# Kernel optimization log

Hardware: AMD Instinct MI355X
Metric: run time of the kernel (lower is better)

The kernel has to match this reference:

```python
import jax, jax.numpy as jnp
import numpy as np

N = 100000          # nodes
E = 1600000         # edges (before self loops)
F_IN = 128          # num_features
HID = 16            # hidden_channels (per head)
HEADS = 4
NCLS = 16           # num_classes (per head)
NEG_SLOPE = 0.2     # PyG GATv2Conv default


def gatv2_conv(x, src, dst, w_l, w_r, att, bias, heads, out_ch):
    """PyG GATv2Conv (concat=True, add_self_loops handled by caller).
    x: [N, Fin]; src/dst: [E']; w_l/w_r: [Fin, heads*out_ch]; att: [heads, out_ch].
    """
    n = x.shape[0]
    x_l = (x @ w_l).reshape(n, heads, out_ch)  # source-side transform
    x_r = (x @ w_r).reshape(n, heads, out_ch)  # target-side transform
    # per-edge attention logits: a^T LeakyReLU(x_l[j] + x_r[i])
    e = jax.nn.leaky_relu(x_l[src] + x_r[dst], NEG_SLOPE)   # [E', H, C]
    logits = jnp.einsum('ehc,hc->eh', e, att)               # [E', H]
    # segment softmax over incoming edges of each dst node
    m = jax.ops.segment_max(logits, dst, num_segments=n)    # [N, H]
    a = jnp.exp(logits - m[dst])
    denom = jax.ops.segment_sum(a, dst, num_segments=n)     # [N, H]
    alpha = a / denom[dst]                                  # self loops => denom > 0
    out = jax.ops.segment_sum(alpha[:, :, None] * x_l[src], dst, num_segments=n)
    return out.reshape(n, heads * out_ch) + bias


def setup_inputs() -> dict:
    key = jax.random.key(0)
    ks = jax.random.split(key, 10)
    x = jax.random.normal(ks[0], (N, F_IN), dtype=jnp.float32)
    edge_index = jax.random.randint(ks[1], (2, E), 0, N, dtype=jnp.int64)
    d1 = HEADS * HID   # 64
    s1 = 1.0 / np.sqrt(F_IN)
    s2 = 1.0 / np.sqrt(d1)
    return {
        'x': x,
        'edge_index': edge_index,
        'w_l1': jax.random.normal(ks[2], (F_IN, d1), dtype=jnp.float32) * s1,
        'w_r1': jax.random.normal(ks[3], (F_IN, d1), dtype=jnp.float32) * s1,
        'att1': jax.random.normal(ks[4], (HEADS, HID), dtype=jnp.float32) * s2,
        'b1': jnp.zeros((d1,), dtype=jnp.float32),
        'w_l2': jax.random.normal(ks[5], (d1, HEADS * NCLS), dtype=jnp.float32) * s2,
        'w_r2': jax.random.normal(ks[6], (d1, HEADS * NCLS), dtype=jnp.float32) * s2,
        'att2': jax.random.normal(ks[7], (HEADS, NCLS), dtype=jnp.float32) * (1.0 / np.sqrt(NCLS)),
        'b2': jnp.zeros((HEADS * NCLS,), dtype=jnp.float32),
    }


def reference(x, edge_index, w_l1, w_r1, att1, b1, w_l2, w_r2, att2, b2):
    # add self loops (PyG GATv2Conv default add_self_loops=True)
    loop = jnp.arange(N, dtype=edge_index.dtype)
    src = jnp.concatenate([edge_index[0], loop])
    dst = jnp.concatenate([edge_index[1], loop])
    h = gatv2_conv(x, src, dst, w_l1, w_r1, att1, b1, HEADS, HID)
    h = jax.nn.relu(h)
    out = gatv2_conv(h, src, dst, w_l2, w_r2, att2, b2, HEADS, NCLS)
    return out
```

## Files before the change

### kernel.cpp

```cpp
#include <hip/hip_runtime.h>
#include <hip/hip_fp16.h>

#define FIN 128
#define BSH 9
#define BMASK ((1 << BSH) - 1)
#define CHUNK 8192
#define BCAP 10240

typedef _Float16 half4 __attribute__((ext_vector_type(4)));
typedef _Float16 h2v __attribute__((ext_vector_type(2)));
typedef float f32x4 __attribute__((ext_vector_type(4)));

static __device__ __forceinline__ float xor1_add(float p) {
  const int sw = __builtin_amdgcn_mov_dpp(__builtin_bit_cast(int, p), 0xB1,
                                          0xF, 0xF, true);
  return p + __builtin_bit_cast(float, sw);
}

template<int K, bool FP32IN>
__global__ __launch_bounds__(256) void gemm_mfma(
    const void* __restrict__ xin, const float* __restrict__ wl,
    const float* __restrict__ wr, __half* __restrict__ outl,
    __half* __restrict__ outr, int n) {
  constexpr int WSTR = K + 4;
  __shared__ _Float16 Wt[128 * WSTR];
  const int tid = threadIdx.x;
  for (int i4 = tid; i4 < K * 16; i4 += 256) {
    const int k = i4 >> 4, c0 = (i4 & 15) << 2;
    const float4 vl = *(const float4*)&wl[k * 64 + c0];
    const float4 vr = *(const float4*)&wr[k * 64 + c0];
    Wt[(c0 + 0) * WSTR + k] = (_Float16)vl.x;
    Wt[(c0 + 1) * WSTR + k] = (_Float16)vl.y;
    Wt[(c0 + 2) * WSTR + k] = (_Float16)vl.z;
    Wt[(c0 + 3) * WSTR + k] = (_Float16)vl.w;
    Wt[(c0 + 64) * WSTR + k] = (_Float16)vr.x;
    Wt[(c0 + 65) * WSTR + k] = (_Float16)vr.y;
    Wt[(c0 + 66) * WSTR + k] = (_Float16)vr.z;
    Wt[(c0 + 67) * WSTR + k] = (_Float16)vr.w;
  }
  __syncthreads();
  const int lane = tid & 63;
  const int wv = tid >> 6;
  const int r0 = blockIdx.x * 64 + wv * 16;
  const int rowc = min(r0 + (lane & 15), n - 1);
  const int kgrp = (lane >> 4) << 2;
  const int col16 = lane & 15;
  f32x4 acc[8];
#pragma unroll
  for (int cf = 0; cf < 8; ++cf) acc[cf] = {0.f, 0.f, 0.f, 0.f};
  for (int ks = 0; ks < K / 16; ++ks) {
    const int kb = ks * 16 + kgrp;
    half4 a;
    if (FP32IN) {
      const float4 av =
          *(const float4*)((const float*)xin + (size_t)rowc * K + kb);
      a = {(_Float16)av.x, (_Float16)av.y, (_Float16)av.z, (_Float16)av.w};
    } else {
      a = *(const half4*)((const __half*)xin + (size_t)rowc * K + kb);
    }
#pragma unroll
    for (int cf = 0; cf < 8; ++cf) {
      const half4 b = *(const half4*)&Wt[(cf * 16 + col16) * WSTR + kb];
      acc[cf] = __builtin_amdgcn_mfma_f32_16x16x16f16(a, b, acc[cf], 0, 0, 0);
    }
  }
  const int crow0 = r0 + ((lane >> 4) << 2);
#pragma unroll
  for (int cf = 0; cf < 8; ++cf) {
    const int c = cf * 16 + col16;
    __half* outp = (c < 64) ? outl : outr;
    const int cc = c & 63;
#pragma unroll
    for (int r = 0; r < 4; ++r) {
      const int rr = crow0 + r;
      if (rr < n) outp[(size_t)rr * 64 + cc] = (__half)acc[cf][r];
    }
  }
}

__global__ __launch_bounds__(256) void binpass(
    const int* __restrict__ src, const int* __restrict__ dst, int E, int ET,
    int NB, int* __restrict__ gcursor, unsigned* __restrict__ sorted_val) {
  __shared__ unsigned lval[CHUNK];
  __shared__ unsigned short lrank[CHUNK];
  __shared__ unsigned char lb[CHUNK];
  __shared__ int c1[256], base[256];
  const int tid = threadIdx.x;
  c1[tid] = 0;
  __syncthreads();
  const int e0 = blockIdx.x * CHUNK;

#define BPROC(idx_, s_, d_)                                                  \
  {                                                                          \
    const int b_ = (d_) >> BSH;                                              \
    lval[idx_] = (unsigned)(s_) | ((unsigned)((d_) & BMASK) << 17);          \
    lb[idx_] = (unsigned char)b_;                                            \
    lrank[idx_] = (unsigned short)atomicAdd(&c1[b_], 1);                     \
  }

#pragma unroll
  for (int j = 0; j < CHUNK / 1024; ++j) {
    const int q = tid + 256 * j;
    const int e = e0 + 4 * q;
    if (e + 3 < E) {
      const int4 s4 = *(const int4*)&src[e];
      const int4 d4 = *(const int4*)&dst[e];
      BPROC(4 * q + 0, s4.x, d4.x);
      BPROC(4 * q + 1, s4.y, d4.y);
      BPROC(4 * q + 2, s4.z, d4.z);
      BPROC(4 * q + 3, s4.w, d4.w);
    } else {
#pragma unroll
      for (int t = 0; t < 4; ++t) {
        const int ee = e + t;
        const int idx = 4 * q + t;
        if (ee < ET) {
          int s, d;
          if (ee < E) {
            s = src[ee];
            d = dst[ee];
          } else {
            s = d = ee - E;
          }
          BPROC(idx, s, d);
        } else {
          lb[idx] = 255;
        }
      }
    }
  }
#undef BPROC
  __syncthreads();
  if (tid < NB && c1[tid] > 0)
    base[tid] = tid * BCAP + atomicAdd(&gcursor[tid], c1[tid]);
  __syncthreads();
#pragma unroll
  for (int j = 0; j < CHUNK / 256; ++j) {
    const int idx = tid + 256 * j;
    const int b = lb[idx];
    if (b != 255) sorted_val[base[b] + lrank[idx]] = lval[idx];
  }
}

__global__ __launch_bounds__(256) void scatter_gemm1(
    const int* __restrict__ gcursor, const unsigned* __restrict__ sorted_val,
    int n, int* __restrict__ ssrc, int2* __restrict__ off2,
    const float* __restrict__ x, const float* __restrict__ wl,
    const float* __restrict__ wr, __half* __restrict__ outl,
    __half* __restrict__ outr, int NB,
    const float* __restrict__ att1, const float* __restrict__ att2,
    __half* __restrict__ att1h, __half* __restrict__ att2h) {
  __shared__ __align__(16) char smem[49152];
  const int tid = threadIdx.x;

  if (blockIdx.x == 0 && tid < 64) {
    att1h[tid] = (__half)(att1[tid] * 1.44269504f);
    att2h[tid] = (__half)(att2[tid] * 1.44269504f);
  }

  if (blockIdx.x < (unsigned)NB) {
    int* cnt = (int*)smem;
    int* sa = cnt + 512;
    int* sb = sa + 512;
    int* cur = sb + 512;
    int* buf = cur + 512;
    const int b = blockIdx.x;
    const int node0 = b << BSH;
    const int nn = min(512, n - node0);
    const int rbase = b * BCAP;
    const int rlen = gcursor[b];
    for (int j = tid; j < 512; j += 256) cnt[j] = 0;
    __syncthreads();
    for (int i = tid; i < rlen; i += 256)
      atomicAdd(&cnt[sorted_val[rbase + i] >> 17], 1);
    __syncthreads();
    for (int j = tid; j < 512; j += 256) sa[j] = cnt[j];
    __syncthreads();
    int* pin = sa;
    int* pout = sb;
    for (int off = 1; off < 512; off <<= 1) {
      for (int j = tid; j < 512; j += 256)
        pout[j] = pin[j] + (j >= off ? pin[j - off] : 0);
      __syncthreads();
      int* t = pin;
      pin = pout;
      pout = t;
    }
    for (int j = tid; j < 512; j += 256) {
      const int excl = pin[j] - cnt[j];
      cur[j] = excl;
      if (j < nn) off2[node0 + j] = make_int2(rbase + excl, rbase + pin[j]);
    }
    __syncthreads();
    if (rlen <= BCAP) {
      for (int i = tid; i < rlen; i += 256) {
        const unsigned v = sorted_val[rbase + i];
        const int p = atomicAdd(&cur[v >> 17], 1);
        buf[p] = (int)(v & 0x1FFFFu);
      }
      __syncthreads();
      for (int i = tid; i < rlen; i += 256) ssrc[rbase + i] = buf[i];
    } else {
      for (int i = tid; i < rlen; i += 256) {
        const unsigned v = sorted_val[rbase + i];
        const int p = atomicAdd(&cur[v >> 17], 1);
        ssrc[rbase + p] = (int)(v & 0x1FFFFu);
      }
    }
  } else {
    constexpr int K = 128;
    constexpr int WSTR = K + 4;
    _Float16* Wt = (_Float16*)smem;
    for (int i4 = tid; i4 < K * 16; i4 += 256) {
      const int k = i4 >> 4, c0 = (i4 & 15) << 2;
      const float4 vl = *(const float4*)&wl[k * 64 + c0];
      const float4 vr = *(const float4*)&wr[k * 64 + c0];
      Wt[(c0 + 0) * WSTR + k] = (_Float16)vl.x;
      Wt[(c0 + 1) * WSTR + k] = (_Float16)vl.y;
      Wt[(c0 + 2) * WSTR + k] = (_Float16)vl.z;
      Wt[(c0 + 3) * WSTR + k] = (_Float16)vl.w;
      Wt[(c0 + 64) * WSTR + k] = (_Float16)vr.x;
      Wt[(c0 + 65) * WSTR + k] = (_Float16)vr.y;
      Wt[(c0 + 66) * WSTR + k] = (_Float16)vr.z;
      Wt[(c0 + 67) * WSTR + k] = (_Float16)vr.w;
    }
    __syncthreads();
    const int lane = tid & 63;
    const int wv = tid >> 6;
    const int r0 = (blockIdx.x - NB) * 64 + wv * 16;
    const int rowc = min(r0 + (lane & 15), n - 1);
    const int kgrp = (lane >> 4) << 2;
    const int col16 = lane & 15;
    f32x4 acc[8];
#pragma unroll
    for (int cf = 0; cf < 8; ++cf) acc[cf] = {0.f, 0.f, 0.f, 0.f};
    for (int ks = 0; ks < K / 16; ++ks) {
      const int kb = ks * 16 + kgrp;
      const float4 av = *(const float4*)&x[(size_t)rowc * K + kb];
      const half4 a = {(_Float16)av.x, (_Float16)av.y, (_Float16)av.z,
                       (_Float16)av.w};
#pragma unroll
      for (int cf = 0; cf < 8; ++cf) {
        const half4 bb = *(const half4*)&Wt[(cf * 16 + col16) * WSTR + kb];
        acc[cf] = __builtin_amdgcn_mfma_f32_16x16x16f16(a, bb, acc[cf], 0, 0, 0);
      }
    }
    const int crow0 = r0 + ((lane >> 4) << 2);
#pragma unroll
    for (int cf = 0; cf < 8; ++cf) {
      const int c = cf * 16 + col16;
      __half* outp = (c < 64) ? outl : outr;
      const int cc = c & 63;
#pragma unroll
      for (int r = 0; r < 4; ++r) {
        const int rr = crow0 + r;
        if (rr < n) outp[(size_t)rr * 64 + cc] = (__half)acc[cf][r];
      }
    }
  }
}

template<bool RELU, typename OT>
__global__ __launch_bounds__(256) void node_pass(
    const int2* __restrict__ off2, const int* __restrict__ ssrc,
    const __half* __restrict__ xl, const __half* __restrict__ xr,
    const __half* __restrict__ atth, const float* __restrict__ bias,
    OT* __restrict__ out, int n) {
  __shared__ float part[4][8][64];
  const int lane = threadIdx.x & 63;
  const int wv = threadIdx.x >> 6;
  const int grp = lane >> 3;
  const int sl = lane & 7;
  const int d = (blockIdx.x * blockDim.x + threadIdx.x) >> 6;
  if (d >= n) return;
  const int2 oo = off2[d];
  const int beg = oo.x, end = oo.y;
  const int deg = end - beg;

  union H8 { float4 f4; h2v h2[4]; uint4 u4; };
  H8 ath;
  ath.u4 = *(const uint4*)&atth[8 * sl];
  H8 xrv;
  xrv.f4 = *(const float4*)&xr[(size_t)d * 64 + 8 * sl];

  h2v acch[4] = {{(_Float16)0.f, (_Float16)0.f},
                 {(_Float16)0.f, (_Float16)0.f},
                 {(_Float16)0.f, (_Float16)0.f},
                 {(_Float16)0.f, (_Float16)0.f}};
  float den = 0.f;

  const unsigned slb = (unsigned)(sl * 16);
  const int sv = ssrc[min(beg + lane, end - 1)];

#define EDGE_CORE(vreg_)                                                     \
  {                                                                          \
    H8 ul;                                                                   \
    ul.f4 = (vreg_);                                                         \
    const h2v t0 = ul.h2[0] + xrv.h2[0];                                     \
    const h2v t1 = ul.h2[1] + xrv.h2[1];                                     \
    const h2v t2 = ul.h2[2] + xrv.h2[2];                                     \
    const h2v t3 = ul.h2[3] + xrv.h2[3];                                     \
    const h2v k0 = __builtin_elementwise_max(t0, t0 * (_Float16)0.2f);       \
    const h2v k1 = __builtin_elementwise_max(t1, t1 * (_Float16)0.2f);       \
    const h2v k2 = __builtin_elementwise_max(t2, t2 * (_Float16)0.2f);       \
    const h2v k3 = __builtin_elementwise_max(t3, t3 * (_Float16)0.2f);       \
    float pa = __builtin_amdgcn_fdot2(k0, ath.h2[0], 0.f, false);            \
    float pb = __builtin_amdgcn_fdot2(k2, ath.h2[2], 0.f, false);            \
    pa = __builtin_amdgcn_fdot2(k1, ath.h2[1], pa, false);                   \
    pb = __builtin_amdgcn_fdot2(k3, ath.h2[3], pb, false);                   \
    const float p = xor1_add(pa + pb);                                       \
    const float a = exp2f(p);                                                \
    const _Float16 ah = (_Float16)a;                                         \
    const h2v aa = {ah, ah};                                                 \
    acch[0] += ul.h2[0] * aa;                                                \
    acch[1] += ul.h2[1] * aa;                                                \
    acch[2] += ul.h2[2] * aa;                                                \
    acch[3] += ul.h2[3] * aa;                                                \
    den += a;                                                                \
  }

  if (deg <= 64) {
#define XLF(base_, dst_)                                                     \
  {                                                                          \
    const int s_ = __shfl(sv, (base_) - beg + grp);                          \
    const unsigned voff_ = (unsigned)s_ * 128u + slb;                        \
    dst_ = *(const float4*)((const char*)xl + voff_);                        \
  }
    float4 a0, a1, nx;
    XLF(beg, a0);
    XLF(beg + 8, a1);
    int base = beg;
#pragma unroll 2
    for (; base + 8 <= end; base += 8) {
      XLF(base + 16, nx);
      EDGE_CORE(a0);
      a0 = a1;
      a1 = nx;
    }
    if (base < end) {
      if (base + grp < end) EDGE_CORE(a0);
    }
#undef XLF
  } else {
#define XLS(base_, dst_)                                                     \
  {                                                                          \
    const int idx_ = (base_) - beg + grp;                                    \
    int s_ = __shfl(sv, idx_ & 63);                                          \
    if (idx_ >= 64) s_ = ssrc[min((base_) + grp, end - 1)];                  \
    const unsigned voff_ = (unsigned)s_ * 128u + slb;                        \
    dst_ = *(const float4*)((const char*)xl + voff_);                        \
  }
    float4 a0, a1, nx;
    XLS(beg, a0);
    XLS(beg + 8, a1);
    for (int base = beg; base < end; base += 8) {
      XLS(base + 16, nx);
      if (base + grp < end) EDGE_CORE(a0);
      a0 = a1;
      a1 = nx;
    }
#undef XLS
  }
#undef EDGE_CORE

#pragma unroll
  for (int m = 8; m <= 32; m <<= 1) den += __shfl_xor(den, m);
  const float den_c = __shfl(den, (lane >> 4) << 1);

  float acc[8];
#pragma unroll
  for (int q = 0; q < 4; ++q) {
    acc[2 * q] = (float)acch[q].x;
    acc[2 * q + 1] = (float)acch[q].y;
  }
  *(float4*)&part[wv][grp][8 * sl] = make_float4(acc[0], acc[1], acc[2], acc[3]);
  *(float4*)&part[wv][grp][8 * sl + 4] =
      make_float4(acc[4], acc[5], acc[6], acc[7]);
  float s = 0.f;
#pragma unroll
  for (int g = 0; g < 8; ++g) s += part[wv][g][lane];

  float v = s / den_c + bias[lane];
  if (RELU) v = fmaxf(v, 0.f);
  out[(size_t)d * 64 + lane] = (OT)v;
}

extern "C" void kernel_launch(void* const* d_in, const int* in_sizes, int n_in,
                              void* d_out, int out_size, void* d_ws, size_t ws_size,
                              hipStream_t stream) {
  const float* x    = (const float*)d_in[0];
  const int*   ei   = (const int*)d_in[1];
  const float* wl1  = (const float*)d_in[2];
  const float* wr1  = (const float*)d_in[3];
  const float* att1 = (const float*)d_in[4];
  const float* b1   = (const float*)d_in[5];
  const float* wl2  = (const float*)d_in[6];
  const float* wr2  = (const float*)d_in[7];
  const float* att2 = (const float*)d_in[8];
  const float* b2   = (const float*)d_in[9];
  float* out = (float*)d_out;

  const int n = in_sizes[0] / FIN;
  const int E = in_sizes[1] / 2;
  const int ET = E + n;
  const int* src = ei;
  const int* dst = ei + E;
  const int NB = (n + (1 << BSH) - 1) >> BSH;

  __half* A  = (__half*)d_ws;
  __half* B  = A + (size_t)n * 64;
  __half* Hh = B + (size_t)n * 64;
  __half* att1h = Hh + (size_t)n * 64;
  __half* att2h = att1h + 64;
  int2* off2 = (int2*)(att2h + 64);
  int* gcursor = (int*)(off2 + n);
  unsigned* sorted_val = (unsigned*)(gcursor + 256);
  int* ssrc = (int*)(sorted_val + (size_t)NB * BCAP);

  const int nbin = (ET + CHUNK - 1) / CHUNK;
  const int gb = (n + 63) / 64;
  const int nb = (n * 64 + 255) / 256;

  hipMemsetAsync(gcursor, 0, 256 * sizeof(int), stream);
  binpass<<<nbin, 256, 0, stream>>>(src, dst, E, ET, NB, gcursor, sorted_val);
  scatter_gemm1<<<NB + gb, 256, 0, stream>>>(
      gcursor, sorted_val, n, ssrc, off2, x, wl1, wr1, A, B, NB, att1, att2,
      att1h, att2h);

  node_pass<true, __half><<<nb, 256, 0, stream>>>(off2, ssrc, A, B, att1h, b1,
                                                  Hh, n);

  gemm_mfma<64, false><<<gb, 256, 0, stream>>>(Hh, wl2, wr2, A, B, n);
  node_pass<false, float><<<nb, 256, 0, stream>>>(off2, ssrc, A, B, att2h, b2,
                                                  out, n);
}
```

Measured before the change: 149.6 us.

## Fuse layer-1 attention aggregation with layer-2 MFMA projection in one kernel

Layer-1 attention aggregation and the layer-2 linear transform now run in one kernel. Each block computes 64 nodes' ReLU outputs into shared memory, then runs the MFMA GEMM on them directly, writing to new C/D buffers. This removes the global hidden-feature round trip and one kernel launch. The trade-off is that each wave processes 16 nodes serially, which reduces the number of concurrent waves available to hide gather latency.

```diff
diff --git a/kernel.cpp b/kernel.cpp
--- a/kernel.cpp
+++ b/kernel.cpp
@@ -11,71 +11,122 @@
 typedef _Float16 h2v __attribute__((ext_vector_type(2)));
 typedef float f32x4 __attribute__((ext_vector_type(4)));
 
+union H8 { float4 f4; h2v h2[4]; uint4 u4; };
+
 static __device__ __forceinline__ float xor1_add(float p) {
   const int sw = __builtin_amdgcn_mov_dpp(__builtin_bit_cast(int, p), 0xB1,
                                           0xF, 0xF, true);
   return p + __builtin_bit_cast(float, sw);
 }
 
-template<int K, bool FP32IN>
-__global__ __launch_bounds__(256) void gemm_mfma(
-    const void* __restrict__ xin, const float* __restrict__ wl,
-    const float* __restrict__ wr, __half* __restrict__ outl,
-    __half* __restrict__ outr, int n) {
-  constexpr int WSTR = K + 4;
-  __shared__ _Float16 Wt[128 * WSTR];
-  const int tid = threadIdx.x;
-  for (int i4 = tid; i4 < K * 16; i4 += 256) {
-    const int k = i4 >> 4, c0 = (i4 & 15) << 2;
-    const float4 vl = *(const float4*)&wl[k * 64 + c0];
-    const float4 vr = *(const float4*)&wr[k * 64 + c0];
-    Wt[(c0 + 0) * WSTR + k] = (_Float16)vl.x;
-    Wt[(c0 + 1) * WSTR + k] = (_Float16)vl.y;
-    Wt[(c0 + 2) * WSTR + k] = (_Float16)vl.z;
-    Wt[(c0 + 3) * WSTR + k] = (_Float16)vl.w;
-    Wt[(c0 + 64) * WSTR + k] = (_Float16)vr.x;
-    Wt[(c0 + 65) * WSTR + k] = (_Float16)vr.y;
-    Wt[(c0 + 66) * WSTR + k] = (_Float16)vr.z;
-    Wt[(c0 + 67) * WSTR + k] = (_Float16)vr.w;
-  }
-  __syncthreads();
-  const int lane = tid & 63;
-  const int wv = tid >> 6;
-  const int r0 = blockIdx.x * 64 + wv * 16;
-  const int rowc = min(r0 + (lane & 15), n - 1);
-  const int kgrp = (lane >> 4) << 2;
-  const int col16 = lane & 15;
-  f32x4 acc[8];
-#pragma unroll
-  for (int cf = 0; cf < 8; ++cf) acc[cf] = {0.f, 0.f, 0.f, 0.f};
-  for (int ks = 0; ks < K / 16; ++ks) {
-    const int kb = ks * 16 + kgrp;
-    half4 a;
-    if (FP32IN) {
-      const float4 av =
-          *(const float4*)((const float*)xin + (size_t)rowc * K + kb);
-      a = {(_Float16)av.x, (_Float16)av.y, (_Float16)av.z, (_Float16)av.w};
-    } else {
-      a = *(const half4*)((const __half*)xin + (size_t)rowc * K + kb);
-    }
-#pragma unroll
-    for (int cf = 0; cf < 8; ++cf) {
-      const half4 b = *(const half4*)&Wt[(cf * 16 + col16) * WSTR + kb];
-      acc[cf] = __builtin_amdgcn_mfma_f32_16x16x16f16(a, b, acc[cf], 0, 0, 0);
-    }
-  }
-  const int crow0 = r0 + ((lane >> 4) << 2);
-#pragma unroll
-  for (int cf = 0; cf < 8; ++cf) {
-    const int c = cf * 16 + col16;
-    __half* outp = (c < 64) ? outl : outr;
-    const int cc = c & 63;
-#pragma unroll
-    for (int r = 0; r < 4; ++r) {
-      const int rr = crow0 + r;
-      if (rr < n) outp[(size_t)rr * 64 + cc] = (__half)acc[cf][r];
-    }
-  }
+static __device__ __forceinline__ float attn_one_node(
+    int d, const int2* __restrict__ off2, const int* __restrict__ ssrc,
+    const __half* __restrict__ xl, const __half* __restrict__ xr,
+    const H8& ath, int lane, int grp, int sl, unsigned slb,
+    float* __restrict__ partw, float biasv) {
+  const int2 oo = off2[d];
+  const int beg = oo.x, end = oo.y;
+  const int deg = end - beg;
+
+  H8 xrv;
+  xrv.f4 = *(const float4*)&xr[(size_t)d * 64 + 8 * sl];
+
+  h2v acch[4] = {{(_Float16)0.f, (_Float16)0.f},
+                 {(_Float16)0.f, (_Float16)0.f},
+                 {(_Float16)0.f, (_Float16)0.f},
+                 {(_Float16)0.f, (_Float16)0.f}};
+  float den = 0.f;
+  const int sv = ssrc[min(beg + lane, end - 1)];
+
+#define EDGE_CORE(vreg_)                                                     \
+  {                                                                          \
+    H8 ul;                                                                   \
+    ul.f4 = (vreg_);                                                         \
+    const h2v t0 = ul.h2[0] + xrv.h2[0];                                     \
+    const h2v t1 = ul.h2[1] + xrv.h2[1];                                     \
+    const h2v t2 = ul.h2[2] + xrv.h2[2];                                     \
+    const h2v t3 = ul.h2[3] + xrv.h2[3];                                     \
+    const h2v k0 = __builtin_elementwise_max(t0, t0 * (_Float16)0.2f);       \
+    const h2v k1 = __builtin_elementwise_max(t1, t1 * (_Float16)0.2f);       \
+    const h2v k2 = __builtin_elementwise_max(t2, t2 * (_Float16)0.2f);       \
+    const h2v k3 = __builtin_elementwise_max(t3, t3 * (_Float16)0.2f);       \
+    float pa = __builtin_amdgcn_fdot2(k0, ath.h2[0], 0.f, false);            \
+    float pb = __builtin_amdgcn_fdot2(k2, ath.h2[2], 0.f, false);            \
+    pa = __builtin_amdgcn_fdot2(k1, ath.h2[1], pa, false);                   \
+    pb = __builtin_amdgcn_fdot2(k3, ath.h2[3], pb, false);                   \
+    const float p = xor1_add(pa + pb);                                       \
+    const float a = exp2f(p);                                                \
+    const _Float16 ah = (_Float16)a;                                         \
+    const h2v aa = {ah, ah};                                                 \
+    acch[0] += ul.h2[0] * aa;                                                \
+    acch[1] += ul.h2[1] * aa;                                                \
+    acch[2] += ul.h2[2] * aa;                                                \
+    acch[3] += ul.h2[3] * aa;                                                \
+    den += a;                                                                \
+  }
+
+  if (deg <= 64) {
+#define XLF(base_, dst_)                                                     \
+  {                                                                          \
+    const int s_ = __shfl(sv, (base_) - beg + grp);                          \
+    const unsigned voff_ = (unsigned)s_ * 128u + slb;                        \
+    dst_ = *(const float4*)((const char*)xl + voff_);                        \
+  }
+    float4 a0, a1, nx;
+    XLF(beg, a0);
+    XLF(beg + 8, a1);
+    int base = beg;
+#pragma unroll 2
+    for (; base + 8 <= end; base += 8) {
+      XLF(base + 16, nx);
+      EDGE_CORE(a0);
+      a0 = a1;
+      a1 = nx;
+    }
+    if (base < end) {
+      if (base + grp < end) EDGE_CORE(a0);
+    }
+#undef XLF
+  } else {
+#define XLS(base_, dst_)                                                     \
+  {                                                                          \
+    const int idx_ = (base_) - beg + grp;                                    \
+    int s_ = __shfl(sv, idx_ & 63);                                          \
+    if (idx_ >= 64) s_ = ssrc[min((base_) + grp, end - 1)];                  \
+    const unsigned voff_ = (unsigned)s_ * 128u + slb;                        \
+    dst_ = *(const float4*)((const char*)xl + voff_);                        \
+  }
+    float4 a0, a1, nx;
+    XLS(beg, a0);
+    XLS(beg + 8, a1);
+    for (int base = beg; base < end; base += 8) {
+      XLS(base + 16, nx);
+      if (base + grp < end) EDGE_CORE(a0);
+      a0 = a1;
+      a1 = nx;
+    }
+#undef XLS
+  }
+#undef EDGE_CORE
+
+#pragma unroll
+  for (int m = 8; m <= 32; m <<= 1) den += __shfl_xor(den, m);
+  const float den_c = __shfl(den, (lane >> 4) << 1);
+
+  float acc[8];
+#pragma unroll
+  for (int q = 0; q < 4; ++q) {
+    acc[2 * q] = (float)acch[q].x;
+    acc[2 * q + 1] = (float)acch[q].y;
+  }
+  *(float4*)&partw[grp * 64 + 8 * sl] =
+      make_float4(acc[0], acc[1], acc[2], acc[3]);
+  *(float4*)&partw[grp * 64 + 8 * sl + 4] =
+      make_float4(acc[4], acc[5], acc[6], acc[7]);
+  float s = 0.f;
+#pragma unroll
+  for (int g = 0; g < 8; ++g) s += partw[g * 64 + lane];
+  return s / den_c + biasv;
 }
 
 __global__ __launch_bounds__(256) void binpass(
@@ -260,12 +311,91 @@
   }
 }
 
-template<bool RELU, typename OT>
-__global__ __launch_bounds__(256) void node_pass(
+__global__ __launch_bounds__(256) void np1_gemm2(
     const int2* __restrict__ off2, const int* __restrict__ ssrc,
     const __half* __restrict__ xl, const __half* __restrict__ xr,
     const __half* __restrict__ atth, const float* __restrict__ bias,
-    OT* __restrict__ out, int n) {
+    const float* __restrict__ wl2, const float* __restrict__ wr2,
+    __half* __restrict__ outl, __half* __restrict__ outr, int n) {
+  constexpr int K = 64;
+  constexpr int WSTR = K + 4;
+  __shared__ __align__(16) char smem[17408 + 64 * 72 * 2];
+  float* part = (float*)smem;
+  _Float16* Wt = (_Float16*)smem;
+  _Float16* Ht = (_Float16*)(smem + 17408);
+
+  const int tid = threadIdx.x;
+  const int lane = tid & 63;
+  const int wv = tid >> 6;
+  const int grp = lane >> 3;
+  const int sl = lane & 7;
+  const unsigned slb = (unsigned)(sl * 16);
+  const int node0 = blockIdx.x * 64;
+
+  H8 ath;
+  ath.u4 = *(const uint4*)&atth[8 * sl];
+  const float biasv = bias[lane];
+  float* partw = part + wv * 8 * 64;
+#pragma unroll 1
+  for (int i = 0; i < 16; ++i) {
+    const int d = node0 + wv * 16 + i;
+    if (d >= n) break;
+    float v = attn_one_node(d, off2, ssrc, xl, xr, ath, lane, grp, sl, slb,
+                            partw, biasv);
+    v = fmaxf(v, 0.f);
+    Ht[(wv * 16 + i) * 72 + lane] = (_Float16)v;
+  }
+  __syncthreads();
+
+  for (int i4 = tid; i4 < K * 16; i4 += 256) {
+    const int k = i4 >> 4, c0 = (i4 & 15) << 2;
+    const float4 vl = *(const float4*)&wl2[k * 64 + c0];
+    const float4 vr = *(const float4*)&wr2[k * 64 + c0];
+    Wt[(c0 + 0) * WSTR + k] = (_Float16)vl.x;
+    Wt[(c0 + 1) * WSTR + k] = (_Float16)vl.y;
+    Wt[(c0 + 2) * WSTR + k] = (_Float16)vl.z;
+    Wt[(c0 + 3) * WSTR + k] = (_Float16)vl.w;
+    Wt[(c0 + 64) * WSTR + k] = (_Float16)vr.x;
+    Wt[(c0 + 65) * WSTR + k] = (_Float16)vr.y;
+    Wt[(c0 + 66) * WSTR + k] = (_Float16)vr.z;
+    Wt[(c0 + 67) * WSTR + k] = (_Float16)vr.w;
+  }
+  __syncthreads();
+
+  const int arow = wv * 16 + (lane & 15);
+  const int kgrp = (lane >> 4) << 2;
+  const int col16 = lane & 15;
+  f32x4 acc[8];
+#pragma unroll
+  for (int cf = 0; cf < 8; ++cf) acc[cf] = {0.f, 0.f, 0.f, 0.f};
+  for (int ks = 0; ks < K / 16; ++ks) {
+    const int kb = ks * 16 + kgrp;
+    const half4 a = *(const half4*)&Ht[arow * 72 + kb];
+#pragma unroll
+    for (int cf = 0; cf < 8; ++cf) {
+      const half4 bb = *(const half4*)&Wt[(cf * 16 + col16) * WSTR + kb];
+      acc[cf] = __builtin_amdgcn_mfma_f32_16x16x16f16(a, bb, acc[cf], 0, 0, 0);
+    }
+  }
+  const int crow0 = node0 + wv * 16 + ((lane >> 4) << 2);
+#pragma unroll
+  for (int cf = 0; cf < 8; ++cf) {
+    const int c = cf * 16 + col16;
+    __half* outp = (c < 64) ? outl : outr;
+    const int cc = c & 63;
+#pragma unroll
+    for (int r = 0; r < 4; ++r) {
+      const int rr = crow0 + r;
+      if (rr < n) outp[(size_t)rr * 64 + cc] = (__half)acc[cf][r];
+    }
+  }
+}
+
+__global__ __launch_bounds__(256) void node_pass2(
+    const int2* __restrict__ off2, const int* __restrict__ ssrc,
+    const __half* __restrict__ xl, const __half* __restrict__ xr,
+    const __half* __restrict__ atth, const float* __restrict__ bias,
+    float* __restrict__ out, int n) {
   __shared__ float part[4][8][64];
   const int lane = threadIdx.x & 63;
   const int wv = threadIdx.x >> 6;
@@ -273,116 +403,12 @@
   const int sl = lane & 7;
   const int d = (blockIdx.x * blockDim.x + threadIdx.x) >> 6;
   if (d >= n) return;
-  const int2 oo = off2[d];
-  const int beg = oo.x, end = oo.y;
-  const int deg = end - beg;
-
-  union H8 { float4 f4; h2v h2[4]; uint4 u4; };
   H8 ath;
   ath.u4 = *(const uint4*)&atth[8 * sl];
-  H8 xrv;
-  xrv.f4 = *(const float4*)&xr[(size_t)d * 64 + 8 * sl];
-
-  h2v acch[4] = {{(_Float16)0.f, (_Float16)0.f},
-                 {(_Float16)0.f, (_Float16)0.f},
-                 {(_Float16)0.f, (_Float16)0.f},
-                 {(_Float16)0.f, (_Float16)0.f}};
-  float den = 0.f;
-
-  const unsigned slb = (unsigned)(sl * 16);
-  const int sv = ssrc[min(beg + lane, end - 1)];
-
-#define EDGE_CORE(vreg_)                                                     \
-  {                                                                          \
-    H8 ul;                                                                   \
-    ul.f4 = (vreg_);                                                         \
-    const h2v t0 = ul.h2[0] + xrv.h2[0];                                     \
-    const h2v t1 = ul.h2[1] + xrv.h2[1];                                     \
-    const h2v t2 = ul.h2[2] + xrv.h2[2];                                     \
-    const h2v t3 = ul.h2[3] + xrv.h2[3];                                     \
-    const h2v k0 = __builtin_elementwise_max(t0, t0 * (_Float16)0.2f);       \
-    const h2v k1 = __builtin_elementwise_max(t1, t1 * (_Float16)0.2f);       \
-    const h2v k2 = __builtin_elementwise_max(t2, t2 * (_Float16)0.2f);       \
-    const h2v k3 = __builtin_elementwise_max(t3, t3 * (_Float16)0.2f);       \
-    float pa = __builtin_amdgcn_fdot2(k0, ath.h2[0], 0.f, false);            \
-    float pb = __builtin_amdgcn_fdot2(k2, ath.h2[2], 0.f, false);            \
-    pa = __builtin_amdgcn_fdot2(k1, ath.h2[1], pa, false);                   \
-    pb = __builtin_amdgcn_fdot2(k3, ath.h2[3], pb, false);                   \
-    const float p = xor1_add(pa + pb);                                       \
-    const float a = exp2f(p);                                                \
-    const _Float16 ah = (_Float16)a;                                         \
-    const h2v aa = {ah, ah};                                                 \
-    acch[0] += ul.h2[0] * aa;                                                \
-    acch[1] += ul.h2[1] * aa;                                                \
-    acch[2] += ul.h2[2] * aa;                                                \
-    acch[3] += ul.h2[3] * aa;                                                \
-    den += a;                                                                \
-  }
-
-  if (deg <= 64) {
-#define XLF(base_, dst_)                                                     \
-  {                                                                          \
-    const int s_ = __shfl(sv, (base_) - beg + grp);                          \
-    const unsigned voff_ = (unsigned)s_ * 128u + slb;                        \
-    dst_ = *(const float4*)((const char*)xl + voff_);                        \
-  }
-    float4 a0, a1, nx;
-    XLF(beg, a0);
-    XLF(beg + 8, a1);
-    int base = beg;
-#pragma unroll 2
-    for (; base + 8 <= end; base += 8) {
-      XLF(base + 16, nx);
-      EDGE_CORE(a0);
-      a0 = a1;
-      a1 = nx;
-    }
-    if (base < end) {
-      if (base + grp < end) EDGE_CORE(a0);
-    }
-#undef XLF
-  } else {
-#define XLS(base_, dst_)                                                     \
-  {                                                                          \
-    const int idx_ = (base_) - beg + grp;                                    \
-    int s_ = __shfl(sv, idx_ & 63);                                          \
-    if (idx_ >= 64) s_ = ssrc[min((base_) + grp, end - 1)];                  \
-    const unsigned voff_ = (unsigned)s_ * 128u + slb;                        \
-    dst_ = *(const float4*)((const char*)xl + voff_);                        \
-  }
-    float4 a0, a1, nx;
-    XLS(beg, a0);
-    XLS(beg + 8, a1);
-    for (int base = beg; base < end; base += 8) {
-      XLS(base + 16, nx);
-      if (base + grp < end) EDGE_CORE(a0);
-      a0 = a1;
-      a1 = nx;
-    }
-#undef XLS
-  }
-#undef EDGE_CORE
-
-#pragma unroll
-  for (int m = 8; m <= 32; m <<= 1) den += __shfl_xor(den, m);
-  const float den_c = __shfl(den, (lane >> 4) << 1);
-
-  float acc[8];
-#pragma unroll
-  for (int q = 0; q < 4; ++q) {
-    acc[2 * q] = (float)acch[q].x;
-    acc[2 * q + 1] = (float)acch[q].y;
-  }
-  *(float4*)&part[wv][grp][8 * sl] = make_float4(acc[0], acc[1], acc[2], acc[3]);
-  *(float4*)&part[wv][grp][8 * sl + 4] =
-      make_float4(acc[4], acc[5], acc[6], acc[7]);
-  float s = 0.f;
-#pragma unroll
-  for (int g = 0; g < 8; ++g) s += part[wv][g][lane];
-
-  float v = s / den_c + bias[lane];
-  if (RELU) v = fmaxf(v, 0.f);
-  out[(size_t)d * 64 + lane] = (OT)v;
+  const float v = attn_one_node(d, off2, ssrc, xl, xr, ath, lane, grp, sl,
+                                (unsigned)(sl * 16), &part[wv][0][0],
+                                bias[lane]);
+  out[(size_t)d * 64 + lane] = v;
 }
 
 extern "C" void kernel_launch(void* const* d_in, const int* in_sizes, int n_in,
@@ -409,8 +435,9 @@
 
   __half* A  = (__half*)d_ws;
   __half* B  = A + (size_t)n * 64;
-  __half* Hh = B + (size_t)n * 64;
-  __half* att1h = Hh + (size_t)n * 64;
+  __half* C  = B + (size_t)n * 64;
+  __half* D  = C + (size_t)n * 64;
+  __half* att1h = D + (size_t)n * 64;
   __half* att2h = att1h + 64;
   int2* off2 = (int2*)(att2h + 64);
   int* gcursor = (int*)(off2 + n);
@@ -427,10 +454,8 @@
       gcursor, sorted_val, n, ssrc, off2, x, wl1, wr1, A, B, NB, att1, att2,
       att1h, att2h);
 
-  node_pass<true, __half><<<nb, 256, 0, stream>>>(off2, ssrc, A, B, att1h, b1,
-                                                  Hh, n);
-
-  gemm_mfma<64, false><<<gb, 256, 0, stream>>>(Hh, wl2, wr2, A, B, n);
-  node_pass<false, float><<<nb, 256, 0, stream>>>(off2, ssrc, A, B, att2h, b2,
-                                                  out, n);
-}
+  np1_gemm2<<<gb, 256, 0, stream>>>(off2, ssrc, A, B, att1h, b1, wl2, wr2, C,
+                                    D, n);
+
+  node_pass2<<<nb, 256, 0, stream>>>(off2, ssrc, C, D, att2h, b2, out, n);
+}
```

Measured after the change: 168.4 us. +12.6%, slower.

## Assign one full head per lane quad, processing 16 edges per wave iteration

Applied to the files above, without the earlier changes.

The node aggregation kernel now gives each lane 16 channels (a whole head) instead of 8. A wave therefore covers 16 edges per step instead of 8, and the cross-lane DPP add for the attention logit is no longer needed. The high-degree path drops the prefetch pipeline in favour of direct index loads. This raises per-lane register use and makes the shared-memory reduction larger (16 partials), and it may reduce memory-level parallelism on high-degree nodes.

```diff
diff --git a/kernel.cpp b/kernel.cpp
--- a/kernel.cpp
+++ b/kernel.cpp
@@ -10,12 +10,6 @@
 typedef _Float16 half4 __attribute__((ext_vector_type(4)));
 typedef _Float16 h2v __attribute__((ext_vector_type(2)));
 typedef float f32x4 __attribute__((ext_vector_type(4)));
-
-static __device__ __forceinline__ float xor1_add(float p) {
-  const int sw = __builtin_amdgcn_mov_dpp(__builtin_bit_cast(int, p), 0xB1,
-                                          0xF, 0xF, true);
-  return p + __builtin_bit_cast(float, sw);
-}
 
 template<int K, bool FP32IN>
 __global__ __launch_bounds__(256) void gemm_mfma(
@@ -266,119 +260,114 @@
     const __half* __restrict__ xl, const __half* __restrict__ xr,
     const __half* __restrict__ atth, const float* __restrict__ bias,
     OT* __restrict__ out, int n) {
-  __shared__ float part[4][8][64];
+  __shared__ float part[4][16][68];
   const int lane = threadIdx.x & 63;
   const int wv = threadIdx.x >> 6;
-  const int grp = lane >> 3;
-  const int sl = lane & 7;
+  const int grp = lane >> 2;
+  const int sl = lane & 3;
   const int d = (blockIdx.x * blockDim.x + threadIdx.x) >> 6;
   if (d >= n) return;
   const int2 oo = off2[d];
   const int beg = oo.x, end = oo.y;
   const int deg = end - beg;
 
-  union H8 { float4 f4; h2v h2[4]; uint4 u4; };
-  H8 ath;
-  ath.u4 = *(const uint4*)&atth[8 * sl];
-  H8 xrv;
-  xrv.f4 = *(const float4*)&xr[(size_t)d * 64 + 8 * sl];
-
-  h2v acch[4] = {{(_Float16)0.f, (_Float16)0.f},
-                 {(_Float16)0.f, (_Float16)0.f},
-                 {(_Float16)0.f, (_Float16)0.f},
-                 {(_Float16)0.f, (_Float16)0.f}};
+  union H16 { float4 f4[2]; h2v h2[8]; uint4 u4[2]; };
+  H16 ath;
+  ath.u4[0] = *(const uint4*)&atth[16 * sl];
+  ath.u4[1] = *(const uint4*)&atth[16 * sl + 8];
+  H16 xrv;
+  xrv.f4[0] = *(const float4*)&xr[(size_t)d * 64 + 16 * sl];
+  xrv.f4[1] = *(const float4*)&xr[(size_t)d * 64 + 16 * sl + 8];
+
+  h2v acch[8] = {{(_Float16)0.f, (_Float16)0.f}, {(_Float16)0.f, (_Float16)0.f},
+                 {(_Float16)0.f, (_Float16)0.f}, {(_Float16)0.f, (_Float16)0.f},
+                 {(_Float16)0.f, (_Float16)0.f}, {(_Float16)0.f, (_Float16)0.f},
+                 {(_Float16)0.f, (_Float16)0.f}, {(_Float16)0.f, (_Float16)0.f}};
   float den = 0.f;
 
-  const unsigned slb = (unsigned)(sl * 16);
+  const unsigned slb = (unsigned)(sl * 32);
   const int sv = ssrc[min(beg + lane, end - 1)];
 
-#define EDGE_CORE(vreg_)                                                     \
+#define EDGE_CORE(lo_, hi_)                                                  \
   {                                                                          \
-    H8 ul;                                                                   \
-    ul.f4 = (vreg_);                                                         \
-    const h2v t0 = ul.h2[0] + xrv.h2[0];                                     \
-    const h2v t1 = ul.h2[1] + xrv.h2[1];                                     \
-    const h2v t2 = ul.h2[2] + xrv.h2[2];                                     \
-    const h2v t3 = ul.h2[3] + xrv.h2[3];                                     \
-    const h2v k0 = __builtin_elementwise_max(t0, t0 * (_Float16)0.2f);       \
-    const h2v k1 = __builtin_elementwise_max(t1, t1 * (_Float16)0.2f);       \
-    const h2v k2 = __builtin_elementwise_max(t2, t2 * (_Float16)0.2f);       \
-    const h2v k3 = __builtin_elementwise_max(t3, t3 * (_Float16)0.2f);       \
-    float pa = __builtin_amdgcn_fdot2(k0, ath.h2[0], 0.f, false);            \
-    float pb = __builtin_amdgcn_fdot2(k2, ath.h2[2], 0.f, false);            \
-    pa = __builtin_amdgcn_fdot2(k1, ath.h2[1], pa, false);                   \
-    pb = __builtin_amdgcn_fdot2(k3, ath.h2[3], pb, false);                   \
-    const float p = xor1_add(pa + pb);                                       \
-    const float a = exp2f(p);                                                \
+    H16 ul;                                                                  \
+    ul.f4[0] = (lo_);                                                        \
+    ul.f4[1] = (hi_);                                                        \
+    float pa = 0.f, pb = 0.f;                                                \
+    _Pragma("unroll") for (int q = 0; q < 4; ++q) {                          \
+      const h2v t = ul.h2[q] + xrv.h2[q];                                    \
+      const h2v lk = __builtin_elementwise_max(t, t * (_Float16)0.2f);       \
+      pa = __builtin_amdgcn_fdot2(lk, ath.h2[q], pa, false);                 \
+    }                                                                        \
+    _Pragma("unroll") for (int q = 4; q < 8; ++q) {                          \
+      const h2v t = ul.h2[q] + xrv.h2[q];                                    \
+      const h2v lk = __builtin_elementwise_max(t, t * (_Float16)0.2f);       \
+      pb = __builtin_amdgcn_fdot2(lk, ath.h2[q], pb, false);                 \
+    }                                                                        \
+    const float a = exp2f(pa + pb);                                          \
     const _Float16 ah = (_Float16)a;                                         \
     const h2v aa = {ah, ah};                                                 \
-    acch[0] += ul.h2[0] * aa;                                                \
-    acch[1] += ul.h2[1] * aa;                                                \
-    acch[2] += ul.h2[2] * aa;                                                \
-    acch[3] += ul.h2[3] * aa;                                                \
+    _Pragma("unroll") for (int q = 0; q < 8; ++q) acch[q] += ul.h2[q] * aa;  \
     den += a;                                                                \
   }
 
   if (deg <= 64) {
-#define XLF(base_, dst_)                                                     \
+#define XLF(base_, lo_, hi_)                                                 \
   {                                                                          \
-    const int s_ = __shfl(sv, (base_) - beg + grp);                          \
+    const int s_ = __shfl(sv, ((base_) - beg + grp) & 63);                   \
     const unsigned voff_ = (unsigned)s_ * 128u + slb;                        \
-    dst_ = *(const float4*)((const char*)xl + voff_);                        \
-  }
-    float4 a0, a1, nx;
-    XLF(beg, a0);
-    XLF(beg + 8, a1);
+    lo_ = *(const float4*)((const char*)xl + voff_);                         \
+    hi_ = *(const float4*)((const char*)xl + voff_ + 16);                    \
+  }
+    float4 a0l, a0h, a1l, a1h, nxl, nxh;
+    XLF(beg, a0l, a0h);
+    XLF(beg + 16, a1l, a1h);
     int base = beg;
 #pragma unroll 2
-    for (; base + 8 <= end; base += 8) {
-      XLF(base + 16, nx);
-      EDGE_CORE(a0);
-      a0 = a1;
-      a1 = nx;
+    for (; base + 16 <= end; base += 16) {
+      XLF(base + 32, nxl, nxh);
+      EDGE_CORE(a0l, a0h);
+      a0l = a1l;
+      a0h = a1h;
+      a1l = nxl;
+      a1h = nxh;
     }
     if (base < end) {
-      if (base + grp < end) EDGE_CORE(a0);
+      if (base + grp < end) EDGE_CORE(a0l, a0h);
     }
 #undef XLF
   } else {
-#define XLS(base_, dst_)                                                     \
-  {                                                                          \
-    const int idx_ = (base_) - beg + grp;                                    \
-    int s_ = __shfl(sv, idx_ & 63);                                          \
-    if (idx_ >= 64) s_ = ssrc[min((base_) + grp, end - 1)];                  \
-    const unsigned voff_ = (unsigned)s_ * 128u + slb;                        \
-    dst_ = *(const float4*)((const char*)xl + voff_);                        \
-  }
-    float4 a0, a1, nx;
-    XLS(beg, a0);
-    XLS(beg + 8, a1);
-    for (int base = beg; base < end; base += 8) {
-      XLS(base + 16, nx);
-      if (base + grp < end) EDGE_CORE(a0);
-      a0 = a1;
-      a1 = nx;
-    }
-#undef XLS
+    for (int base = beg; base < end; base += 16) {
+      if (base + grp < end) {
+        const int s_ = ssrc[base + grp];
+        const unsigned voff_ = (unsigned)s_ * 128u + slb;
+        const float4 lo = *(const float4*)((const char*)xl + voff_);
+        const float4 hi = *(const float4*)((const char*)xl + voff_ + 16);
+        EDGE_CORE(lo, hi);
+      }
+    }
   }
 #undef EDGE_CORE
 
 #pragma unroll
-  for (int m = 8; m <= 32; m <<= 1) den += __shfl_xor(den, m);
-  const float den_c = __shfl(den, (lane >> 4) << 1);
-
-  float acc[8];
-#pragma unroll
-  for (int q = 0; q < 4; ++q) {
-    acc[2 * q] = (float)acch[q].x;
-    acc[2 * q + 1] = (float)acch[q].y;
-  }
-  *(float4*)&part[wv][grp][8 * sl] = make_float4(acc[0], acc[1], acc[2], acc[3]);
-  *(float4*)&part[wv][grp][8 * sl + 4] =
-      make_float4(acc[4], acc[5], acc[6], acc[7]);
+  for (int m = 4; m <= 32; m <<= 1) den += __shfl_xor(den, m);
+  const float den_c = __shfl(den, lane >> 4);
+
+  float accf[16];
+#pragma unroll
+  for (int q = 0; q < 8; ++q) {
+    accf[2 * q] = (float)acch[q].x;
+    accf[2 * q + 1] = (float)acch[q].y;
+  }
+  float* pw = &part[wv][grp][16 * sl];
+#pragma unroll
+  for (int q = 0; q < 4; ++q)
+    *(float4*)&pw[4 * q] =
+        make_float4(accf[4 * q], accf[4 * q + 1], accf[4 * q + 2],
+                    accf[4 * q + 3]);
   float s = 0.f;
 #pragma unroll
-  for (int g = 0; g < 8; ++g) s += part[wv][g][lane];
+  for (int g = 0; g < 16; ++g) s += part[wv][g][lane];
 
   float v = s / den_c + bias[lane];
   if (RELU) v = fmaxf(v, 0.f);
```

New measurement: 159.1 us. 6.4% more time.
